# Kernel optimization log

Measured on AMD Instinct MI355X. Metric: run time of the kernel, lower is better.

## Reference

```python
import jax, jax.numpy as jnp
import numpy as np


def setup_inputs() -> dict:
    key = jax.random.key(0)
    k1, k2 = jax.random.split(key)
    B, S, K, N = 2, 4096, 4096, 4096
    x = jax.random.randint(k1, (B, S, K), -127, 128, dtype=jnp.int32).astype(jnp.int8)
    weight = jax.random.randint(k2, (N, K), -127, 128, dtype=jnp.int32).astype(jnp.int8)
    bias = jnp.zeros((1, N), dtype=jnp.int8)
    a = jnp.float32(0.01)   # alpha = input_scale * weight_scale / output_scale
    b = jnp.float32(1.0)    # beta = bias_scale / output_scale
    return {"x": x, "weight": weight, "bias": bias, "a": a, "b": b}


def reference(x, weight, bias, a, b):
    # i8gemm.linear_a8_w8_b8_o8: int8 GEMM with int32 accumulation, then
    # y_int8 = saturate_cast(round(alpha * acc + beta * bias)).
    x_shape = x.shape
    xf = x.reshape(-1, x_shape[-1])                     # [M, K] int8
    acc = jnp.matmul(xf, weight.T, preferred_element_type=jnp.int32)  # [M, N]
    y = a * acc.astype(jnp.float32) + b * bias.astype(jnp.float32)    # fused epilogue
    yq = jnp.clip(jnp.round(y), -128.0, 127.0).astype(jnp.int8)       # requantize o8
    return yq.reshape(*x_shape[:-1], -1)
```

## Files before the change

### kernel.cpp

```cpp
#include <hip/hip_runtime.h>
#include <stdint.h>

#define M_DIM 8192
#define N_DIM 4096
#define K_DIM 4096

using int4v = __attribute__((ext_vector_type(4))) int;

__global__ __launch_bounds__(256) void pack_kernel(const int4* __restrict__ sx,
                                                   const int4* __restrict__ sw,
                                                   unsigned int* __restrict__ dst,
                                                   int nx, int ntot) {
    int idx = blockIdx.x * blockDim.x + threadIdx.x;
    if (idx >= ntot) return;
    int4 v = (idx < nx) ? sx[idx] : sw[idx - nx];
    dst[idx] = (v.x & 0xff) | ((v.y & 0xff) << 8) | ((v.z & 0xff) << 16) |
               ((v.w & 0xff) << 24);
}

__device__ __forceinline__ void async_copy16(const char* g, char* l) {
    __builtin_amdgcn_global_load_lds(
        (const __attribute__((address_space(1))) char*)g,
        (__attribute__((address_space(3))) char*)l, 16, 0, 0);
}

__global__ __launch_bounds__(512, 2) void gemm_i8_kernel(
    const char* __restrict__ Aq,
    const char* __restrict__ Bq,
    const int* __restrict__ bias,
    const float* __restrict__ a_ptr,
    const float* __restrict__ b_ptr,
    int32_t* __restrict__ out)
{
    __shared__ char As0[256 * 128];
    __shared__ char As1[256 * 128];
    __shared__ char Bs0[256 * 128];
    __shared__ char Bs1[256 * 128];

    const int tid  = threadIdx.x;
    const int lane = tid & 63;
    const int wave = tid >> 6;
    const int wr   = wave >> 2;
    const int wc   = wave & 3;

    const int bid = blockIdx.x;
    const int xcd = bid & 7;
    const int lin = bid >> 3;
    const int m0  = ((xcd & 3) * 8 + (lin & 7)) * 256;
    const int n0  = ((xcd >> 2) * 8 + (lin >> 3)) * 256;

    const float alpha = *a_ptr;
    const float beta  = *b_ptr;

    int4v acc[8][4] = {};

    const int fr = lane & 15;
    const int gw = lane >> 4;
    const int swz = (fr >> 1) & 7;
    const int k0off = (gw ^ swz) << 4;
    const int k1off = ((4 + gw) ^ swz) << 4;
    const int arow = wr * 128 + fr;
    const int brow = wc * 64 + fr;

    const int srow = tid >> 3;
    const int scg  = ((tid & 7) ^ ((tid >> 4) & 7)) << 4;
    const char* gA0 = Aq + (size_t)(m0 + srow) * K_DIM + scg;
    const char* gA1 = gA0 + (size_t)64 * K_DIM;
    const char* gB0 = Bq + (size_t)(n0 + srow) * K_DIM + scg;
    const char* gB1 = gB0 + (size_t)64 * K_DIM;

#define STAGE_A(AS, h, t)                                                    \
    {                                                                        \
        const size_t off_ = (size_t)(h) * (128 * K_DIM) + (size_t)(t) * 128; \
        char* l_ = &AS[(h)*16384 + (tid << 4)];                              \
        async_copy16(gA0 + off_, l_);                                        \
        async_copy16(gA1 + off_, l_ + 8192);                                 \
    }

#define STAGE_B(BS, h, t)                                                    \
    {                                                                        \
        const size_t off_ = (size_t)(h) * (128 * K_DIM) + (size_t)(t) * 128; \
        char* l_ = &BS[(h)*16384 + (tid << 4)];                              \
        async_copy16(gB0 + off_, l_);                                        \
        async_copy16(gB1 + off_, l_ + 8192);                                 \
    }

#define STAGE_TILE(AS, BS, t)                                                \
    {                                                                        \
        STAGE_A(AS, 0, t);                                                   \
        STAGE_A(AS, 1, t);                                                   \
        STAGE_B(BS, 0, t);                                                   \
        STAGE_B(BS, 1, t);                                                   \
    }

#define DS_A2(AS, qm)                                                        \
    {                                                                        \
        _Pragma("unroll") for (int ii = 0; ii < 4; ++ii) {                   \
            const char* pa_ = &AS[(arow + ((qm)*4 + ii) * 16) * 128];        \
            af[ii * 2 + 0] = *(const int4v*)(pa_ + k0off);                   \
            af[ii * 2 + 1] = *(const int4v*)(pa_ + k1off);                   \
        }                                                                    \
    }

#define DS_B2(BS, R, qn)                                                     \
    {                                                                        \
        _Pragma("unroll") for (int jj = 0; jj < 2; ++jj) {                   \
            const char* pb_ = &BS[(brow + ((qn)*2 + jj) * 16) * 128];        \
            R[jj * 2 + 0] = *(const int4v*)(pb_ + k0off);                    \
            R[jj * 2 + 1] = *(const int4v*)(pb_ + k1off);                    \
        }                                                                    \
    }

#define MM2(qm, qn, RB)                                                      \
    {                                                                        \
        _Pragma("unroll") for (int ii = 0; ii < 4; ++ii)                     \
        _Pragma("unroll") for (int jj = 0; jj < 2; ++jj)                     \
        _Pragma("unroll") for (int kk = 0; kk < 2; ++kk)                     \
            acc[(qm)*4 + ii][(qn)*2 + jj] =                                  \
                __builtin_amdgcn_mfma_i32_16x16x64_i8(                       \
                    af[ii * 2 + kk], RB[jj * 2 + kk],                        \
                    acc[(qm)*4 + ii][(qn)*2 + jj], 0, 0, 0);                 \
    }

#define COMPUTE_TILE(AS, BS)                                                 \
    {                                                                        \
        int4v af[8], bf0[4], bf1[4];                                         \
        DS_A2(AS, 0);                                                        \
        DS_B2(BS, bf0, 0);                                                   \
        DS_B2(BS, bf1, 1);                                                   \
        __builtin_amdgcn_s_setprio(1);                                       \
        MM2(0, 0, bf0);                                                      \
        MM2(0, 1, bf1);                                                      \
        DS_A2(AS, 1);                                                        \
        MM2(1, 0, bf0);                                                      \
        MM2(1, 1, bf1);                                                      \
        __builtin_amdgcn_s_setprio(0);                                       \
    }

#define TILE_END                                                             \
    {                                                                        \
        asm volatile("s_waitcnt vmcnt(0)" ::: "memory");                     \
        __builtin_amdgcn_s_barrier();                                        \
        __builtin_amdgcn_sched_barrier(0);                                   \
    }

    STAGE_TILE(As0, Bs0, 0);
    TILE_END;

#pragma unroll 1
    for (int it = 0; it < 15; ++it) {
        const int t1 = 2 * it + 1;
        const int t2 = 2 * it + 2;
        STAGE_TILE(As1, Bs1, t1);
        __builtin_amdgcn_sched_barrier(0);
        COMPUTE_TILE(As0, Bs0);
        TILE_END;
        STAGE_TILE(As0, Bs0, t2);
        __builtin_amdgcn_sched_barrier(0);
        COMPUTE_TILE(As1, Bs1);
        TILE_END;
    }
    STAGE_TILE(As1, Bs1, 31);
    __builtin_amdgcn_sched_barrier(0);
    COMPUTE_TILE(As0, Bs0);
    TILE_END;
    COMPUTE_TILE(As1, Bs1);

    const int orow = (lane >> 4) * 4;
    const int ocol = lane & 15;
#pragma unroll
    for (int j = 0; j < 4; ++j) {
        const int gn = n0 + wc * 64 + j * 16 + ocol;
        const float bb = beta * (float)bias[gn];
#pragma unroll
        for (int i = 0; i < 8; ++i) {
            const int gm = m0 + wr * 128 + i * 16 + orow;
#pragma unroll
            for (int r = 0; r < 4; ++r) {
                float v = alpha * (float)acc[i][j][r] + bb;
                v = rintf(v);
                v = fminf(fmaxf(v, -128.0f), 127.0f);
                out[(size_t)(gm + r) * N_DIM + gn] = (int32_t)v;
            }
        }
    }
}

extern "C" void kernel_launch(void* const* d_in, const int* in_sizes, int n_in,
                              void* d_out, int out_size, void* d_ws, size_t ws_size,
                              hipStream_t stream) {
    const int*   x    = (const int*)d_in[0];
    const int*   w    = (const int*)d_in[1];
    const int*   bias = (const int*)d_in[2];
    const float* a    = (const float*)d_in[3];
    const float* b    = (const float*)d_in[4];
    int32_t*     out  = (int32_t*)d_out;

    char* xq = (char*)d_ws;
    const int nx   = (M_DIM * K_DIM) / 4;
    const int nw   = (N_DIM * K_DIM) / 4;
    const int ntot = nx + nw;
    pack_kernel<<<(ntot + 255) / 256, 256, 0, stream>>>(
        (const int4*)x, (const int4*)w, (unsigned int*)xq, nx, ntot);

    char* wq = xq + (size_t)M_DIM * K_DIM;

    dim3 grid((M_DIM / 256) * (N_DIM / 256));
    gemm_i8_kernel<<<grid, 512, 0, stream>>>(xq, wq, bias, a, b, out);
}
```

Before: 394.9 us.

## Switch int8 GEMM to 32x32x32 MFMA tiles with wave-staggered A loads

Replaces the 16x16x64 int8 MFMA micro-tiles with 32x32x32 MFMAs, which changes the accumulator layout to 4x2 blocks of 16 ints, and reworks the LDS fragment addressing and the epilogue row mapping to match. Odd and even waves walk the A sub-tiles in opposite order, which is meant to spread LDS bank traffic and keep MFMA issue busy. The larger MFMA cuts instruction count and fragment reload traffic. In exchange the register pressure pattern changes and the epilogue stores are spread across more rows.

```diff
diff --git a/kernel.cpp b/kernel.cpp
--- a/kernel.cpp
+++ b/kernel.cpp
@@ -5,7 +5,8 @@
 #define N_DIM 4096
 #define K_DIM 4096
 
-using int4v = __attribute__((ext_vector_type(4))) int;
+using int4v  = __attribute__((ext_vector_type(4))) int;
+using int16v = __attribute__((ext_vector_type(16))) int;
 
 __global__ __launch_bounds__(256) void pack_kernel(const int4* __restrict__ sx,
                                                    const int4* __restrict__ sw,
@@ -46,21 +47,25 @@
     const int bid = blockIdx.x;
     const int xcd = bid & 7;
     const int lin = bid >> 3;
-    const int m0  = ((xcd & 3) * 8 + (lin & 7)) * 256;
-    const int n0  = ((xcd >> 2) * 8 + (lin >> 3)) * 256;
+    const int tile_m = (xcd & 3) * 8 + (lin & 7);
+    const int tile_n = (xcd >> 2) * 8 + (lin >> 3);
+    const int m0 = tile_m * 256;
+    const int n0 = tile_n * 256;
 
     const float alpha = *a_ptr;
     const float beta  = *b_ptr;
 
-    int4v acc[8][4] = {};
-
-    const int fr = lane & 15;
-    const int gw = lane >> 4;
-    const int swz = (fr >> 1) & 7;
-    const int k0off = (gw ^ swz) << 4;
-    const int k1off = ((4 + gw) ^ swz) << 4;
-    const int arow = wr * 128 + fr;
-    const int brow = wc * 64 + fr;
+    int16v acc[4][2] = {};
+
+    const int al  = lane & 31;
+    const int kg  = lane >> 5;
+    const int key = (al >> 1) & 7;
+    int koff[4];
+#pragma unroll
+    for (int ks = 0; ks < 4; ++ks)
+        koff[ks] = ((ks * 2 + kg) ^ key) << 4;
+    const int abase = (wr * 128 + al) * 128;
+    const int bbase = (wc * 64 + al) * 128;
 
     const int srow = tid >> 3;
     const int scg  = ((tid & 7) ^ ((tid >> 4) & 7)) << 4;
@@ -69,72 +74,72 @@
     const char* gB0 = Bq + (size_t)(n0 + srow) * K_DIM + scg;
     const char* gB1 = gB0 + (size_t)64 * K_DIM;
 
-#define STAGE_A(AS, h, t)                                                    \
-    {                                                                        \
-        const size_t off_ = (size_t)(h) * (128 * K_DIM) + (size_t)(t) * 128; \
-        char* l_ = &AS[(h)*16384 + (tid << 4)];                              \
-        async_copy16(gA0 + off_, l_);                                        \
-        async_copy16(gA1 + off_, l_ + 8192);                                 \
-    }
-
-#define STAGE_B(BS, h, t)                                                    \
-    {                                                                        \
-        const size_t off_ = (size_t)(h) * (128 * K_DIM) + (size_t)(t) * 128; \
-        char* l_ = &BS[(h)*16384 + (tid << 4)];                              \
-        async_copy16(gB0 + off_, l_);                                        \
-        async_copy16(gB1 + off_, l_ + 8192);                                 \
-    }
-
 #define STAGE_TILE(AS, BS, t)                                                \
     {                                                                        \
-        STAGE_A(AS, 0, t);                                                   \
-        STAGE_A(AS, 1, t);                                                   \
-        STAGE_B(BS, 0, t);                                                   \
-        STAGE_B(BS, 1, t);                                                   \
-    }
-
-#define DS_A2(AS, qm)                                                        \
-    {                                                                        \
-        _Pragma("unroll") for (int ii = 0; ii < 4; ++ii) {                   \
-            const char* pa_ = &AS[(arow + ((qm)*4 + ii) * 16) * 128];        \
-            af[ii * 2 + 0] = *(const int4v*)(pa_ + k0off);                   \
-            af[ii * 2 + 1] = *(const int4v*)(pa_ + k1off);                   \
+        const size_t offL = (size_t)(t) * 128;                               \
+        const size_t offH = (size_t)128 * K_DIM + (size_t)(t) * 128;         \
+        async_copy16(gA0 + offL, &AS[(tid << 4)]);                           \
+        async_copy16(gA1 + offL, &AS[(tid << 4) + 8192]);                    \
+        async_copy16(gA0 + offH, &AS[16384 + (tid << 4)]);                   \
+        async_copy16(gA1 + offH, &AS[16384 + (tid << 4) + 8192]);            \
+        async_copy16(gB0 + offL, &BS[(tid << 4)]);                           \
+        async_copy16(gB1 + offL, &BS[(tid << 4) + 8192]);                    \
+        async_copy16(gB0 + offH, &BS[16384 + (tid << 4)]);                   \
+        async_copy16(gB1 + offH, &BS[16384 + (tid << 4) + 8192]);            \
+    }
+
+#define LOAD_A(AS, AF, mt)                                                   \
+    _Pragma("unroll") for (int ks = 0; ks < 4; ++ks)                         \
+        AF[ks] = *(const int4v*)&AS[abase + (mt)*4096 + koff[ks]];
+
+#define LOAD_B(BS, BF, nt)                                                   \
+    _Pragma("unroll") for (int ks = 0; ks < 4; ++ks)                         \
+        BF[ks] = *(const int4v*)&BS[bbase + (nt)*4096 + koff[ks]];
+
+#define MMH(mlo, A0, A1)                                                     \
+    {                                                                        \
+        __builtin_amdgcn_s_setprio(1);                                       \
+        _Pragma("unroll") for (int ks = 0; ks < 4; ++ks) {                   \
+            acc[(mlo)][0] = __builtin_amdgcn_mfma_i32_32x32x32_i8(           \
+                A0[ks], bf0[ks], acc[(mlo)][0], 0, 0, 0);                    \
+            acc[(mlo)][1] = __builtin_amdgcn_mfma_i32_32x32x32_i8(           \
+                A0[ks], bf1[ks], acc[(mlo)][1], 0, 0, 0);                    \
+            acc[(mlo) + 1][0] = __builtin_amdgcn_mfma_i32_32x32x32_i8(       \
+                A1[ks], bf0[ks], acc[(mlo) + 1][0], 0, 0, 0);                \
+            acc[(mlo) + 1][1] = __builtin_amdgcn_mfma_i32_32x32x32_i8(       \
+                A1[ks], bf1[ks], acc[(mlo) + 1][1], 0, 0, 0);                \
         }                                                                    \
-    }
-
-#define DS_B2(BS, R, qn)                                                     \
-    {                                                                        \
-        _Pragma("unroll") for (int jj = 0; jj < 2; ++jj) {                   \
-            const char* pb_ = &BS[(brow + ((qn)*2 + jj) * 16) * 128];        \
-            R[jj * 2 + 0] = *(const int4v*)(pb_ + k0off);                    \
-            R[jj * 2 + 1] = *(const int4v*)(pb_ + k1off);                    \
+        __builtin_amdgcn_s_setprio(0);                                       \
+    }
+
+#define COMPUTE_TILE(AS, BS)                                                 \
+    {                                                                        \
+        int4v bf0[4], bf1[4];                                                \
+        LOAD_B(BS, bf0, 0);                                                  \
+        LOAD_B(BS, bf1, 1);                                                  \
+        if (wave & 1) {                                                      \
+            {                                                                \
+                int4v a0[4], a1[4];                                          \
+                LOAD_A(AS, a0, 2); LOAD_A(AS, a1, 3);                        \
+                MMH(2, a0, a1);                                              \
+            }                                                                \
+            {                                                                \
+                int4v a0[4], a1[4];                                          \
+                LOAD_A(AS, a0, 0); LOAD_A(AS, a1, 1);                        \
+                MMH(0, a0, a1);                                              \
+            }                                                                \
+        } else {                                                             \
+            {                                                                \
+                int4v a0[4], a1[4];                                          \
+                LOAD_A(AS, a0, 0); LOAD_A(AS, a1, 1);                        \
+                MMH(0, a0, a1);                                              \
+            }                                                                \
+            {                                                                \
+                int4v a0[4], a1[4];                                          \
+                LOAD_A(AS, a0, 2); LOAD_A(AS, a1, 3);                        \
+                MMH(2, a0, a1);                                              \
+            }                                                                \
         }                                                                    \
-    }
-
-#define MM2(qm, qn, RB)                                                      \
-    {                                                                        \
-        _Pragma("unroll") for (int ii = 0; ii < 4; ++ii)                     \
-        _Pragma("unroll") for (int jj = 0; jj < 2; ++jj)                     \
-        _Pragma("unroll") for (int kk = 0; kk < 2; ++kk)                     \
-            acc[(qm)*4 + ii][(qn)*2 + jj] =                                  \
-                __builtin_amdgcn_mfma_i32_16x16x64_i8(                       \
-                    af[ii * 2 + kk], RB[jj * 2 + kk],                        \
-                    acc[(qm)*4 + ii][(qn)*2 + jj], 0, 0, 0);                 \
-    }
-
-#define COMPUTE_TILE(AS, BS)                                                 \
-    {                                                                        \
-        int4v af[8], bf0[4], bf1[4];                                         \
-        DS_A2(AS, 0);                                                        \
-        DS_B2(BS, bf0, 0);                                                   \
-        DS_B2(BS, bf1, 1);                                                   \
-        __builtin_amdgcn_s_setprio(1);                                       \
-        MM2(0, 0, bf0);                                                      \
-        MM2(0, 1, bf1);                                                      \
-        DS_A2(AS, 1);                                                        \
-        MM2(1, 0, bf0);                                                      \
-        MM2(1, 1, bf1);                                                      \
-        __builtin_amdgcn_s_setprio(0);                                       \
     }
 
 #define TILE_END                                                             \
@@ -149,13 +154,11 @@
 
 #pragma unroll 1
     for (int it = 0; it < 15; ++it) {
-        const int t1 = 2 * it + 1;
-        const int t2 = 2 * it + 2;
-        STAGE_TILE(As1, Bs1, t1);
+        STAGE_TILE(As1, Bs1, 2 * it + 1);
         __builtin_amdgcn_sched_barrier(0);
         COMPUTE_TILE(As0, Bs0);
         TILE_END;
-        STAGE_TILE(As0, Bs0, t2);
+        STAGE_TILE(As0, Bs0, 2 * it + 2);
         __builtin_amdgcn_sched_barrier(0);
         COMPUTE_TILE(As1, Bs1);
         TILE_END;
@@ -166,21 +169,21 @@
     TILE_END;
     COMPUTE_TILE(As1, Bs1);
 
-    const int orow = (lane >> 4) * 4;
-    const int ocol = lane & 15;
-#pragma unroll
-    for (int j = 0; j < 4; ++j) {
-        const int gn = n0 + wc * 64 + j * 16 + ocol;
+    const int obr = kg * 4;
+#pragma unroll
+    for (int nt = 0; nt < 2; ++nt) {
+        const int gn = n0 + wc * 64 + nt * 32 + al;
         const float bb = beta * (float)bias[gn];
 #pragma unroll
-        for (int i = 0; i < 8; ++i) {
-            const int gm = m0 + wr * 128 + i * 16 + orow;
-#pragma unroll
-            for (int r = 0; r < 4; ++r) {
-                float v = alpha * (float)acc[i][j][r] + bb;
+        for (int mt = 0; mt < 4; ++mt) {
+            const int gmb = m0 + wr * 128 + mt * 32 + obr;
+#pragma unroll
+            for (int reg = 0; reg < 16; ++reg) {
+                const int gm = gmb + (reg & 3) + 8 * (reg >> 2);
+                float v = alpha * (float)acc[mt][nt][reg] + bb;
                 v = rintf(v);
                 v = fminf(fmaxf(v, -128.0f), 127.0f);
-                out[(size_t)(gm + r) * N_DIM + gn] = (int32_t)v;
+                out[(size_t)gm * N_DIM + gn] = (int32_t)v;
             }
         }
     }
```

After: 454.4 us. +15.1%, slower.
